# Kernel tuning notes

Hardware: AMD Instinct MI355X
Metric: run time of the kernel (lower is better)

The kernel has to match this reference:

```python
import jax, jax.numpy as jnp
import numpy as np

N, D, H, F = 50000, 128, 8, 512
HD = D // H
EPS_BN = 1e-5


def _batchnorm(x, gamma, beta):
    # BatchNorm1d in training mode: per-feature batch stats over node dim
    m = x.mean(axis=0)
    v = x.var(axis=0)
    return (x - m) * jax.lax.rsqrt(v + EPS_BN) * gamma + beta


def setup_inputs() -> dict:
    key = jax.random.key(0)
    ks = jax.random.split(key, 12)
    s = 0.05
    return {
        "src": jax.random.normal(ks[0], (N, D), jnp.float32),
        "edge_index": jax.random.randint(ks[1], (2, 800000), 0, N, jnp.int64),
        "q_w": jax.random.normal(ks[2], (D, D), jnp.float32) * s,
        "q_b": jnp.zeros((D,), jnp.float32),
        "k_w": jax.random.normal(ks[3], (D, D), jnp.float32) * s,
        "v_w": jax.random.normal(ks[4], (D, D), jnp.float32) * s,
        "out_w": jax.random.normal(ks[5], (D, D), jnp.float32) * s,
        "out_b": jnp.zeros((D,), jnp.float32),
        "g1": jnp.ones((D,), jnp.float32),
        "b1": jnp.zeros((D,), jnp.float32),
        "lin1_w": jax.random.normal(ks[6], (F, D), jnp.float32) * s,
        "lin1_b": jnp.zeros((F,), jnp.float32),
        "lin2_w": jax.random.normal(ks[7], (D, F), jnp.float32) * s,
        "lin2_b": jnp.zeros((D,), jnp.float32),
        "g2": jnp.ones((D,), jnp.float32),
        "b2": jnp.zeros((D,), jnp.float32),
    }


def reference(src, edge_index, q_w, q_b, k_w, v_w, out_w, out_b,
              g1, b1, lin1_w, lin1_b, lin2_w, lin2_b, g2, b2):
    n = src.shape[0]
    # add self loops, then attention edge index is (dst=edge[1], src=edge[0])
    loops = jnp.arange(n, dtype=edge_index.dtype)
    ei = jnp.concatenate([edge_index, jnp.stack([loops, loops])], axis=1)
    e_src, e_dst = ei[0], ei[1]  # message flows e_src -> e_dst; query index = e_dst

    scaling = float(HD) ** (-0.5)
    q = ((src @ q_w.T + q_b) * scaling).reshape(n, H, HD)
    k = (src @ k_w.T).reshape(n, H, HD)
    v = (src @ v_w.T).reshape(n, H, HD)

    # per-edge scores [E, H]
    w = jnp.einsum("ehd,ehd->eh", q[e_dst], k[e_src])
    # deterministic segment softmax over edges grouped by destination node
    mx = jax.ops.segment_max(w, e_dst, num_segments=n)
    ex = jnp.exp(w - mx[e_dst])
    den = jax.ops.segment_sum(ex, e_dst, num_segments=n)
    attn_w = ex / (den[e_dst] + 1e-16)  # [E, H]

    # weighted scatter-add aggregation -> [n, H, HD]
    msgs = attn_w[:, :, None] * v[e_src]
    agg = jax.ops.segment_sum(msgs, e_dst, num_segments=n)

    attn_out = agg.reshape(n, D) @ out_w.T + out_b
    x = _batchnorm(src + attn_out, g1, b1)

    ff = jax.nn.leaky_relu(x @ lin1_w.T + lin1_b, negative_slope=0.01)
    ff = ff @ lin2_w.T + lin2_b
    x = _batchnorm(x + ff, g2, b2)
    return x
```

## Files before the change

kernel.cpp:

```cpp
#include <hip/hip_runtime.h>
#include <math.h>

#define D 128
#define H 8
#define HD 16

typedef __attribute__((ext_vector_type(8))) short bf16x8;
typedef __attribute__((ext_vector_type(4))) float f32x4;

__device__ __forceinline__ ushort f2bf(float x) {
    union { float f; unsigned u; } v; v.f = x;
    unsigned r = v.u + 0x7fffu + ((v.u >> 16) & 1u);
    return (ushort)(r >> 16);
}
__device__ __forceinline__ float bflo(unsigned u) {
    union { unsigned u; float f; } x; x.u = u << 16; return x.f;
}
__device__ __forceinline__ float bfhi(unsigned u) {
    union { unsigned u; float f; } x; x.u = u & 0xffff0000u; return x.f;
}
__device__ __forceinline__ float bf2f(short s) {
    union { unsigned u; float f; } x; x.u = ((unsigned)(ushort)s) << 16; return x.f;
}

__device__ __forceinline__ float dot16(const float* qf, uint4 a, uint4 b) {
    float w;
    w  = qf[0]  * bflo(a.x) + qf[1]  * bfhi(a.x);
    w += qf[2]  * bflo(a.y) + qf[3]  * bfhi(a.y);
    w += qf[4]  * bflo(a.z) + qf[5]  * bfhi(a.z);
    w += qf[6]  * bflo(a.w) + qf[7]  * bfhi(a.w);
    w += qf[8]  * bflo(b.x) + qf[9]  * bfhi(b.x);
    w += qf[10] * bflo(b.y) + qf[11] * bfhi(b.y);
    w += qf[12] * bflo(b.z) + qf[13] * bfhi(b.z);
    w += qf[14] * bflo(b.w) + qf[15] * bfhi(b.w);
    return w;
}
__device__ __forceinline__ void acc16(float* num, float e, uint4 a, uint4 b) {
    num[0]  = fmaf(e, bflo(a.x), num[0]);  num[1]  = fmaf(e, bfhi(a.x), num[1]);
    num[2]  = fmaf(e, bflo(a.y), num[2]);  num[3]  = fmaf(e, bfhi(a.y), num[3]);
    num[4]  = fmaf(e, bflo(a.z), num[4]);  num[5]  = fmaf(e, bfhi(a.z), num[5]);
    num[6]  = fmaf(e, bflo(a.w), num[6]);  num[7]  = fmaf(e, bfhi(a.w), num[7]);
    num[8]  = fmaf(e, bflo(b.x), num[8]);  num[9]  = fmaf(e, bfhi(b.x), num[9]);
    num[10] = fmaf(e, bflo(b.y), num[10]); num[11] = fmaf(e, bfhi(b.y), num[11]);
    num[12] = fmaf(e, bflo(b.z), num[12]); num[13] = fmaf(e, bfhi(b.z), num[13]);
    num[14] = fmaf(e, bflo(b.w), num[14]); num[15] = fmaf(e, bfhi(b.w), num[15]);
}

template<int EPI, int M, int STATS>
__global__ __launch_bounds__(256)
void gemm_v4_kernel(const ushort* __restrict__ A,
                    const ushort* __restrict__ W,
                    const float* __restrict__ bias,
                    const float* __restrict__ extf,
                    ushort* __restrict__ outb,
                    float* __restrict__ stats,
                    int N)
{
    const int lane = threadIdx.x & 63, wave = threadIdx.x >> 6;
    const int lr = lane & 15, lq = lane >> 4;
    const int colbase = blockIdx.y * 128 + wave * 32;

    bf16x8 bfr[2][4];
    {
        const ushort* wp = W + (size_t)(colbase + lr) * 128 + lq * 8;
        #pragma unroll
        for (int ct = 0; ct < 2; ++ct)
            #pragma unroll
            for (int t = 0; t < 4; ++t)
                bfr[ct][t] = *(const bf16x8*)(wp + (size_t)ct * 16 * 128 + t * 32);
    }
    float biasv[2];
    biasv[0] = bias[colbase + lr];
    biasv[1] = bias[colbase + 16 + lr];

    float ssum[2] = {0.f, 0.f}, ssq[2] = {0.f, 0.f};

    const int stride = gridDim.x * 32;
    int r0 = blockIdx.x * 32;
    if (r0 < N) {
        bf16x8 cur[2][4], nxt[2][4];
        auto loadA = [&](int rb, bf16x8 (&dst)[2][4]) {
            #pragma unroll
            for (int s = 0; s < 2; ++s) {
                int ar = min(rb + s * 16 + lr, N - 1);
                const ushort* ap = A + (size_t)ar * 128 + lq * 8;
                #pragma unroll
                for (int t = 0; t < 4; ++t)
                    dst[s][t] = *(const bf16x8*)(ap + t * 32);
            }
        };
        loadA(r0, cur);

        while (true) {
            int rn = r0 + stride;
            if (rn < N) loadA(rn, nxt);

            f32x4 acc[2][2] = {};
            #pragma unroll
            for (int t = 0; t < 4; ++t) {
                acc[0][0] = __builtin_amdgcn_mfma_f32_16x16x32_bf16(cur[0][t], bfr[0][t], acc[0][0], 0, 0, 0);
                acc[1][0] = __builtin_amdgcn_mfma_f32_16x16x32_bf16(cur[1][t], bfr[0][t], acc[1][0], 0, 0, 0);
                acc[0][1] = __builtin_amdgcn_mfma_f32_16x16x32_bf16(cur[0][t], bfr[1][t], acc[0][1], 0, 0, 0);
                acc[1][1] = __builtin_amdgcn_mfma_f32_16x16x32_bf16(cur[1][t], bfr[1][t], acc[1][1], 0, 0, 0);
            }

            #pragma unroll
            for (int ct = 0; ct < 2; ++ct) {
                int gcol = colbase + ct * 16 + lr;
                #pragma unroll
                for (int s = 0; s < 2; ++s) {
                    #pragma unroll
                    for (int r = 0; r < 4; ++r) {
                        int grow = r0 + s * 16 + lq * 4 + r;
                        if (grow >= N) continue;
                        size_t o = (size_t)grow * M + gcol;
                        float v = acc[s][ct][r] + biasv[ct];
                        if (EPI == 2)      v = v > 0.f ? v : 0.01f * v;
                        else if (EPI == 3) v += extf[o];
                        if (STATS) { ssum[ct] += v; ssq[ct] = fmaf(v, v, ssq[ct]); }
                        outb[o] = f2bf(v);
                    }
                }
            }

            if (rn >= N) break;
            r0 = rn;
            #pragma unroll
            for (int s = 0; s < 2; ++s)
                #pragma unroll
                for (int t = 0; t < 4; ++t) cur[s][t] = nxt[s][t];
        }
    }

    if (STATS) {
        #pragma unroll
        for (int ct = 0; ct < 2; ++ct) {
            float a = ssum[ct], b = ssq[ct];
            a += __shfl_xor(a, 16, 64);  b += __shfl_xor(b, 16, 64);
            a += __shfl_xor(a, 32, 64);  b += __shfl_xor(b, 32, 64);
            if (lq == 0) {
                unsafeAtomicAdd(&stats[colbase + ct * 16 + lr], a);
                unsafeAtomicAdd(&stats[128 + colbase + ct * 16 + lr], b);
            }
        }
    }
}

#define LIN2_MFMA4(buf, kcb) \
    acc[0] = __builtin_amdgcn_mfma_f32_16x16x32_bf16(buf[0][0], bfr[(kcb)*4+0], acc[0], 0, 0, 0); \
    acc[1] = __builtin_amdgcn_mfma_f32_16x16x32_bf16(buf[1][0], bfr[(kcb)*4+0], acc[1], 0, 0, 0); \
    acc[0] = __builtin_amdgcn_mfma_f32_16x16x32_bf16(buf[0][1], bfr[(kcb)*4+1], acc[0], 0, 0, 0); \
    acc[1] = __builtin_amdgcn_mfma_f32_16x16x32_bf16(buf[1][1], bfr[(kcb)*4+1], acc[1], 0, 0, 0); \
    acc[0] = __builtin_amdgcn_mfma_f32_16x16x32_bf16(buf[0][2], bfr[(kcb)*4+2], acc[0], 0, 0, 0); \
    acc[1] = __builtin_amdgcn_mfma_f32_16x16x32_bf16(buf[1][2], bfr[(kcb)*4+2], acc[1], 0, 0, 0); \
    acc[0] = __builtin_amdgcn_mfma_f32_16x16x32_bf16(buf[0][3], bfr[(kcb)*4+3], acc[0], 0, 0, 0); \
    acc[1] = __builtin_amdgcn_mfma_f32_16x16x32_bf16(buf[1][3], bfr[(kcb)*4+3], acc[1], 0, 0, 0);

template<int GX>
__global__ __launch_bounds__(256, 3)
void lin2_kernel(const ushort* __restrict__ Ap,
                 const ushort* __restrict__ W,
                 const float* __restrict__ bias,
                 const ushort* __restrict__ extb,
                 const float* __restrict__ rawstats,
                 const float* __restrict__ gg,
                 const float* __restrict__ bb,
                 ushort* __restrict__ outb,
                 float* __restrict__ stats2,
                 int N)
{
    const int lane = threadIdx.x & 63, wave = threadIdx.x >> 6;
    const int lr = lane & 15, lq = lane >> 4;
    const int col = blockIdx.y * 64 + wave * 16 + lr;

    bf16x8 bfr[16];
    {
        const ushort* wp = W + (size_t)col * 512 + lq * 8;
        #pragma unroll
        for (int t = 0; t < 16; ++t) bfr[t] = *(const bf16x8*)(wp + t * 32);
    }
    float biasv = bias[col];
    float mean = rawstats[col] / (float)N;
    float var  = rawstats[128 + col] / (float)N - mean * mean;
    float scv  = gg[col] * rsqrtf(var + 1e-5f);
    float shv  = bb[col] - mean * scv;

    float ssum = 0.f, ssq = 0.f;

    const int stride = GX * 32;
    int r0 = blockIdx.x * 32;
    if (r0 < N) {
        bf16x8 bufA[2][4], bufB[2][4];
        auto loadA = [&](int rb, int kc, bf16x8 (&dst)[2][4]) {
            #pragma unroll
            for (int s = 0; s < 2; ++s) {
                int ar = min(rb + s * 16 + lr, N - 1);
                const ushort* ap = Ap + (size_t)ar * 512 + kc * 128 + lq * 8;
                #pragma unroll
                for (int t = 0; t < 4; ++t)
                    dst[s][t] = *(const bf16x8*)(ap + t * 32);
            }
        };
        loadA(r0, 0, bufA);
        while (true) {
            int rn = r0 + stride;
            f32x4 acc[2] = {};
            loadA(r0, 1, bufB);
            LIN2_MFMA4(bufA, 0)
            loadA(r0, 2, bufA);
            LIN2_MFMA4(bufB, 1)
            loadA(r0, 3, bufB);
            LIN2_MFMA4(bufA, 2)
            if (rn < N) loadA(rn, 0, bufA);
            LIN2_MFMA4(bufB, 3)

            #pragma unroll
            for (int s = 0; s < 2; ++s) {
                #pragma unroll
                for (int r = 0; r < 4; ++r) {
                    int grow = r0 + s * 16 + lq * 4 + r;
                    if (grow >= N) continue;
                    size_t o = (size_t)grow * 128 + col;
                    float v = acc[s][r] + biasv + fmaf(bf2f((short)extb[o]), scv, shv);
                    ssum += v;
                    ssq = fmaf(v, v, ssq);
                    outb[o] = f2bf(v);
                }
            }
            if (rn >= N) break;
            r0 = rn;
        }
    }
    ssum += __shfl_xor(ssum, 16, 64);
    ssq  += __shfl_xor(ssq, 16, 64);
    ssum += __shfl_xor(ssum, 32, 64);
    ssq  += __shfl_xor(ssq, 32, 64);
    if (lq == 0) {
        unsafeAtomicAdd(&stats2[col], ssum);
        unsafeAtomicAdd(&stats2[128 + col], ssq);
    }
}

__global__ __launch_bounds__(256)
void convert_deg_kernel(const float* __restrict__ qw, const float* __restrict__ qb,
                        const float* __restrict__ kw, const float* __restrict__ vw,
                        const float* __restrict__ ow, const float* __restrict__ w1,
                        const float* __restrict__ w2,
                        ushort* __restrict__ wqkv, ushort* __restrict__ wout,
                        ushort* __restrict__ w1b, ushort* __restrict__ w2b,
                        float* __restrict__ bqkv,
                        const float* __restrict__ src, ushort* __restrict__ srcbf,
                        int nd8,
                        const int* __restrict__ ei, long long E0,
                        int* __restrict__ deg)
{
    long long i = (long long)blockIdx.x * 256 + threadIdx.x;
    if (i < E0) atomicAdd(&deg[ei[E0 + i]], 1);
    if (i < nd8) {
        const float4* sp = (const float4*)(src + i * 8);
        float4 f0 = sp[0], f1 = sp[1];
        ushort u[8];
        u[0]=f2bf(f0.x); u[1]=f2bf(f0.y); u[2]=f2bf(f0.z); u[3]=f2bf(f0.w);
        u[4]=f2bf(f1.x); u[5]=f2bf(f1.y); u[6]=f2bf(f1.z); u[7]=f2bf(f1.w);
        *(uint4*)(srcbf + i * 8) = *(uint4*)u;
    }
    if (i < 49152) {
        int row = (int)i >> 7;
        float v;
        if (row < 128)      v = 0.25f * qw[i];
        else if (row < 256) v = kw[i - 16384];
        else                v = vw[i - 32768];
        wqkv[i] = f2bf(v);
        return;
    }
    long long j = i - 49152;
    if (j < 16384) { wout[j] = f2bf(ow[j]); return; }
    j -= 16384;
    if (j < 65536) { w1b[j] = f2bf(w1[j]); return; }
    j -= 65536;
    if (j < 65536) { w2b[j] = f2bf(w2[j]); return; }
    j -= 65536;
    if (j < 384) bqkv[j] = (j < 128) ? 0.25f * qb[j] : 0.f;
}

__global__ __launch_bounds__(256)
void w1fold_kernel(const ushort* __restrict__ w1b, const float* __restrict__ lb1,
                   const float* __restrict__ rawstats,
                   const float* __restrict__ g1, const float* __restrict__ b1,
                   ushort* __restrict__ w1f, float* __restrict__ bias1f, int N)
{
    int f = blockIdx.x * 4 + (threadIdx.x >> 6);
    int lane = threadIdx.x & 63;
    int k0 = lane * 2;
    float m0 = rawstats[k0] / (float)N;
    float v0 = rawstats[128 + k0] / (float)N - m0 * m0;
    float sc0 = g1[k0] * rsqrtf(v0 + 1e-5f);
    float sh0 = b1[k0] - m0 * sc0;
    float m1 = rawstats[k0 + 1] / (float)N;
    float v1 = rawstats[128 + k0 + 1] / (float)N - m1 * m1;
    float sc1 = g1[k0 + 1] * rsqrtf(v1 + 1e-5f);
    float sh1 = b1[k0 + 1] - m1 * sc1;

    uint wp = *(const uint*)(w1b + (size_t)f * 128 + k0);
    float w0 = bflo(wp), w1v = bfhi(wp);
    uint o = (uint)f2bf(w0 * sc0) | ((uint)f2bf(w1v * sc1) << 16);
    *(uint*)(w1f + (size_t)f * 128 + k0) = o;

    float part = w0 * sh0 + w1v * sh1;
    #pragma unroll
    for (int m = 1; m < 64; m <<= 1) part += __shfl_xor(part, m, 64);
    if (lane == 0) bias1f[f] = lb1[f] + part;
}

__global__ __launch_bounds__(256)
void scan_block_sum(const int* __restrict__ deg, int n, int* __restrict__ bsum)
{
    __shared__ int sh[256];
    int i = blockIdx.x * 256 + threadIdx.x;
    sh[threadIdx.x] = (i < n) ? deg[i] : 0;
    __syncthreads();
    for (int ofs = 128; ofs > 0; ofs >>= 1) {
        if (threadIdx.x < ofs) sh[threadIdx.x] += sh[threadIdx.x + ofs];
        __syncthreads();
    }
    if (threadIdx.x == 0) bsum[blockIdx.x] = sh[0];
}

__global__ __launch_bounds__(256)
void scan_final(const int* __restrict__ deg, int n, const int* __restrict__ bsum,
                int nb, int* __restrict__ rowptr)
{
    __shared__ int sb[256];
    __shared__ int sh[256];
    int t = threadIdx.x;
    sb[t] = (t < nb) ? bsum[t] : 0;
    __syncthreads();
    for (int ofs = 1; ofs < 256; ofs <<= 1) {
        int v = (t >= ofs) ? sb[t - ofs] : 0;
        __syncthreads();
        sb[t] += v;
        __syncthreads();
    }
    int boff = (blockIdx.x == 0) ? 0 : sb[blockIdx.x - 1];

    int i = blockIdx.x * 256 + t;
    int v = (i < n) ? deg[i] : 0;
    sh[t] = v;
    __syncthreads();
    for (int ofs = 1; ofs < 256; ofs <<= 1) {
        int u = (t >= ofs) ? sh[t - ofs] : 0;
        __syncthreads();
        sh[t] += u;
        __syncthreads();
    }
    if (i < n) rowptr[i] = boff + sh[t] - v;
    if (i == n - 1) rowptr[n] = boff + sh[t];
}

__global__ __launch_bounds__(256)
void scatter_kernel(const int* __restrict__ ei, long long E0,
                    const int* __restrict__ rowptr, int* __restrict__ cnt,
                    int* __restrict__ col)
{
    long long e = (long long)blockIdx.x * 256 + threadIdx.x;
    if (e >= E0) return;
    int s = ei[e], d = ei[E0 + e];
    int pos = rowptr[d] + atomicAdd(&cnt[d], 1);
    col[pos] = s;
}

__global__ __launch_bounds__(256)
void gat_agg_kernel(const int* __restrict__ rowptr, const int* __restrict__ col,
                    const ushort* __restrict__ qkv, ushort* __restrict__ agg, int N)
{
    int node = blockIdx.x * 4 + (threadIdx.x >> 6);
    if (node >= N) return;
    int lane = threadIdx.x & 63;
    int es = lane >> 3, h = lane & 7;
    const uint4* Q = (const uint4*)qkv;

    const uint4* qp = Q + (size_t)node * 48 + h * 2;
    uint4 qa = qp[0], qb = qp[1];
    float qf[16];
    qf[0]=bflo(qa.x); qf[1]=bfhi(qa.x); qf[2]=bflo(qa.y); qf[3]=bfhi(qa.y);
    qf[4]=bflo(qa.z); qf[5]=bfhi(qa.z); qf[6]=bflo(qa.w); qf[7]=bfhi(qa.w);
    qf[8]=bflo(qb.x); qf[9]=bfhi(qb.x); qf[10]=bflo(qb.y); qf[11]=bfhi(qb.y);
    qf[12]=bflo(qb.z); qf[13]=bfhi(qb.z); qf[14]=bflo(qb.w); qf[15]=bfhi(qb.w);

    float num[16];
    #pragma unroll
    for (int i = 0; i < 16; i++) num[i] = 0.f;
    float den = 0.f;

    int beg = rowptr[node];
    int total = rowptr[node + 1] - beg + 1;
    for (int idx = es; idx < total; idx += 8) {
        int s = (idx == 0) ? node : col[beg + idx - 1];
        const uint4* rp = Q + (size_t)s * 48 + h * 2;
        uint4 ka = rp[16], kb = rp[17], va = rp[32], vb = rp[33];
        float ev = __expf(dot16(qf, ka, kb));
        den += ev;
        acc16(num, ev, va, vb);
    }

    #pragma unroll
    for (int m = 8; m < 64; m <<= 1) {
        den += __shfl_xor(den, m, 64);
        #pragma unroll
        for (int i = 0; i < 16; i++) num[i] += __shfl_xor(num[i], m, 64);
    }

    if (es == 0) {
        float inv = 1.f / (den + 1e-16f);
        uint4 o0, o1;
        o0.x = (uint)f2bf(num[0]*inv)  | ((uint)f2bf(num[1]*inv)  << 16);
        o0.y = (uint)f2bf(num[2]*inv)  | ((uint)f2bf(num[3]*inv)  << 16);
        o0.z = (uint)f2bf(num[4]*inv)  | ((uint)f2bf(num[5]*inv)  << 16);
        o0.w = (uint)f2bf(num[6]*inv)  | ((uint)f2bf(num[7]*inv)  << 16);
        o1.x = (uint)f2bf(num[8]*inv)  | ((uint)f2bf(num[9]*inv)  << 16);
        o1.y = (uint)f2bf(num[10]*inv) | ((uint)f2bf(num[11]*inv) << 16);
        o1.z = (uint)f2bf(num[12]*inv) | ((uint)f2bf(num[13]*inv) << 16);
        o1.w = (uint)f2bf(num[14]*inv) | ((uint)f2bf(num[15]*inv) << 16);
        uint4* op = (uint4*)(agg + (size_t)node * 128 + h * 16);
        op[0] = o0; op[1] = o1;
    }
}

__global__ __launch_bounds__(256)
void bn_apply_out_kernel(const ushort* __restrict__ y, const float* __restrict__ rawstats,
                         const float* __restrict__ g, const float* __restrict__ b,
                         float* __restrict__ out, int total4, int N)
{
    __shared__ float scs[128], shs[128];
    if (threadIdx.x < 128) {
        int j = threadIdx.x;
        float mean = rawstats[j] / (float)N;
        float var  = rawstats[128 + j] / (float)N - mean * mean;
        float sc = g[j] * rsqrtf(var + 1e-5f);
        scs[j] = sc;
        shs[j] = b[j] - mean * sc;
    }
    __syncthreads();
    int i = blockIdx.x * 256 + threadIdx.x;
    if (i >= total4) return;
    uint2 u = reinterpret_cast<const uint2*>(y)[i];
    int j = (i * 4) & (D - 1);
    float4 v;
    v.x = bflo(u.x) * scs[j + 0] + shs[j + 0];
    v.y = bfhi(u.x) * scs[j + 1] + shs[j + 1];
    v.z = bflo(u.y) * scs[j + 2] + shs[j + 2];
    v.w = bfhi(u.y) * scs[j + 3] + shs[j + 3];
    reinterpret_cast<float4*>(out)[i] = v;
}

extern "C" void kernel_launch(void* const* d_in, const int* in_sizes, int n_in,
                              void* d_out, int out_size, void* d_ws, size_t ws_size,
                              hipStream_t stream)
{
    const float* src    = (const float*)d_in[0];
    const int*   ei     = (const int*)  d_in[1];
    const float* q_w    = (const float*)d_in[2];
    const float* q_b    = (const float*)d_in[3];
    const float* k_w    = (const float*)d_in[4];
    const float* v_w    = (const float*)d_in[5];
    const float* out_w  = (const float*)d_in[6];
    const float* out_b  = (const float*)d_in[7];
    const float* g1     = (const float*)d_in[8];
    const float* b1     = (const float*)d_in[9];
    const float* lin1_w = (const float*)d_in[10];
    const float* lin1_b = (const float*)d_in[11];
    const float* lin2_w = (const float*)d_in[12];
    const float* lin2_b = (const float*)d_in[13];
    const float* g2     = (const float*)d_in[14];
    const float* b2     = (const float*)d_in[15];

    const int N        = in_sizes[0] / D;
    const long long E0 = in_sizes[1] / 2;

    float* ws = (float*)d_ws;
    size_t off = 0;
    ushort* qkv   = (ushort*)(ws + off); off += (size_t)N * 192;
    ushort* agg   = (ushort*)(ws + off); off += (size_t)N * 64;
    ushort* srcbf = (ushort*)(ws + off); off += (size_t)N * 64;
    ushort* y1b   = (ushort*)(ws + off); off += (size_t)N * 64;
    ushort* hid   = (ushort*)(ws + off); off += (size_t)N * 256;
    ushort* y2b   = (ushort*)(ws + off); off += (size_t)N * 64;
    ushort* wqkv  = (ushort*)(ws + off); off += 24576;
    ushort* woutb = (ushort*)(ws + off); off += 8192;
    ushort* w1b   = (ushort*)(ws + off); off += 32768;
    ushort* w1f   = (ushort*)(ws + off); off += 32768;
    ushort* w2b   = (ushort*)(ws + off); off += 32768;
    float*  bqkv  = ws + off;            off += 384;
    float*  bias1f= ws + off;            off += 512;
    size_t zero_start = off;
    int* deg    = (int*)(ws + off); off += N;
    int* cnt    = (int*)(ws + off); off += N;
    float* stats1 = ws + off; off += 512;
    float* stats2 = ws + off; off += 512;
    size_t zero_cnt = off - zero_start;
    int* rowptr = (int*)(ws + off); off += N + 1;
    int* bsum   = (int*)(ws + off); off += 256;
    int* col    = (int*)(ws + off); off += E0;

    hipMemsetAsync(ws + zero_start, 0, zero_cnt * sizeof(float), stream);

    dim3 blk(256);

    dim3 gE0((unsigned)((E0 + 255) / 256));
    hipLaunchKernelGGL(convert_deg_kernel, gE0, blk, 0, stream,
                       q_w, q_b, k_w, v_w, out_w, lin1_w, lin2_w,
                       wqkv, woutb, w1b, w2b, bqkv,
                       src, srcbf, N * 16, ei, E0, deg);

    int nb = (N + 255) / 256;
    hipLaunchKernelGGL(scan_block_sum, dim3(nb), blk, 0, stream, deg, N, bsum);
    hipLaunchKernelGGL(scan_final, dim3(nb), blk, 0, stream, deg, N, bsum, nb, rowptr);
    hipLaunchKernelGGL(scatter_kernel, gE0, blk, 0, stream, ei, E0, rowptr, cnt, col);

    const int gx = 1024;

    hipLaunchKernelGGL((gemm_v4_kernel<0, 384, 0>), dim3(gx, 3), blk, 0, stream,
                       srcbf, wqkv, bqkv, nullptr, qkv, nullptr, N);

    hipLaunchKernelGGL(gat_agg_kernel, dim3((N + 3) / 4), blk, 0, stream,
                       rowptr, col, qkv, agg, N);

    hipLaunchKernelGGL((gemm_v4_kernel<3, 128, 1>), dim3(gx, 1), blk, 0, stream,
                       agg, woutb, out_b, src, y1b, stats1, N);

    hipLaunchKernelGGL(w1fold_kernel, dim3(128), blk, 0, stream,
                       w1b, lin1_b, stats1, g1, b1, w1f, bias1f, N);

    hipLaunchKernelGGL((gemm_v4_kernel<2, 512, 0>), dim3(gx, 4), blk, 0, stream,
                       y1b, w1f, bias1f, nullptr, hid, nullptr, N);

    hipLaunchKernelGGL((lin2_kernel<512>), dim3(512, 2), blk, 0, stream,
                       hid, w2b, lin2_b, y1b, stats1, g1, b1, y2b, stats2, N);

    int total4 = N * D / 4;
    hipLaunchKernelGGL(bn_apply_out_kernel, dim3((total4 + 255) / 256), blk, 0, stream,
                       y2b, stats2, g2, b2, (float*)d_out, total4, N);
}
```

Baseline: 448.6 us.

## Fuse FFN lin1 and lin2 GEMMs into one kernel keeping hidden in registers

Replaces the separate lin1 GEMM, which wrote a bf16 hidden tensor of size N×512, and the lin2 kernel with a single fused kernel. Each wave takes 32 rows, computes 32-wide hidden slices with MFMA, applies bias and leaky ReLU, repacks the result to bf16 with permlane swaps, and feeds it straight into the lin2 MFMAs. The BN1 residual, BN2 statistics and output write are folded into the epilogue. This removes the hidden tensor round trip through HBM and one launch, but each wave now reloads the W1 and W2 fragments from global memory or cache, and register pressure is higher (64 accumulator VGPRs per wave, occupancy bound of 2).

After: 545.7 us. 21.6% more time.

```diff
diff --git a/kernel.cpp b/kernel.cpp
--- a/kernel.cpp
+++ b/kernel.cpp
@@ -146,98 +146,153 @@
     }
 }
 
-#define LIN2_MFMA4(buf, kcb) \
-    acc[0] = __builtin_amdgcn_mfma_f32_16x16x32_bf16(buf[0][0], bfr[(kcb)*4+0], acc[0], 0, 0, 0); \
-    acc[1] = __builtin_amdgcn_mfma_f32_16x16x32_bf16(buf[1][0], bfr[(kcb)*4+0], acc[1], 0, 0, 0); \
-    acc[0] = __builtin_amdgcn_mfma_f32_16x16x32_bf16(buf[0][1], bfr[(kcb)*4+1], acc[0], 0, 0, 0); \
-    acc[1] = __builtin_amdgcn_mfma_f32_16x16x32_bf16(buf[1][1], bfr[(kcb)*4+1], acc[1], 0, 0, 0); \
-    acc[0] = __builtin_amdgcn_mfma_f32_16x16x32_bf16(buf[0][2], bfr[(kcb)*4+2], acc[0], 0, 0, 0); \
-    acc[1] = __builtin_amdgcn_mfma_f32_16x16x32_bf16(buf[1][2], bfr[(kcb)*4+2], acc[1], 0, 0, 0); \
-    acc[0] = __builtin_amdgcn_mfma_f32_16x16x32_bf16(buf[0][3], bfr[(kcb)*4+3], acc[0], 0, 0, 0); \
-    acc[1] = __builtin_amdgcn_mfma_f32_16x16x32_bf16(buf[1][3], bfr[(kcb)*4+3], acc[1], 0, 0, 0);
-
-template<int GX>
-__global__ __launch_bounds__(256, 3)
-void lin2_kernel(const ushort* __restrict__ Ap,
-                 const ushort* __restrict__ W,
-                 const float* __restrict__ bias,
-                 const ushort* __restrict__ extb,
-                 const float* __restrict__ rawstats,
-                 const float* __restrict__ gg,
-                 const float* __restrict__ bb,
-                 ushort* __restrict__ outb,
-                 float* __restrict__ stats2,
-                 int N)
-{
+__global__ __launch_bounds__(256, 2)
+void ffn_fused_kernel(const ushort* __restrict__ y1b,
+                      const ushort* __restrict__ w1f,
+                      const float*  __restrict__ bias1f,
+                      const ushort* __restrict__ w2b,
+                      const float*  __restrict__ lb2,
+                      const float*  __restrict__ rawstats,
+                      const float*  __restrict__ g1b,
+                      const float*  __restrict__ b1b,
+                      ushort* __restrict__ y2b,
+                      float*  __restrict__ stats2,
+                      int N)
+{
+    __shared__ float scs[128], adv[128], b1s[512];
+    {
+        int t = threadIdx.x;
+        if (t < 128) {
+            float mean = rawstats[t] / (float)N;
+            float var  = rawstats[128 + t] / (float)N - mean * mean;
+            float sc = g1b[t] * rsqrtf(var + 1e-5f);
+            scs[t] = sc;
+            adv[t] = lb2[t] + b1b[t] - mean * sc;
+        }
+        b1s[t] = bias1f[t];
+        b1s[t + 256] = bias1f[t + 256];
+    }
+    __syncthreads();
+
     const int lane = threadIdx.x & 63, wave = threadIdx.x >> 6;
     const int lr = lane & 15, lq = lane >> 4;
-    const int col = blockIdx.y * 64 + wave * 16 + lr;
-
-    bf16x8 bfr[16];
-    {
-        const ushort* wp = W + (size_t)col * 512 + lq * 8;
-        #pragma unroll
-        for (int t = 0; t < 16; ++t) bfr[t] = *(const bf16x8*)(wp + t * 32);
-    }
-    float biasv = bias[col];
-    float mean = rawstats[col] / (float)N;
-    float var  = rawstats[128 + col] / (float)N - mean * mean;
-    float scv  = gg[col] * rsqrtf(var + 1e-5f);
-    float shv  = bb[col] - mean * scv;
-
-    float ssum = 0.f, ssq = 0.f;
-
-    const int stride = GX * 32;
-    int r0 = blockIdx.x * 32;
-    if (r0 < N) {
-        bf16x8 bufA[2][4], bufB[2][4];
-        auto loadA = [&](int rb, int kc, bf16x8 (&dst)[2][4]) {
-            #pragma unroll
-            for (int s = 0; s < 2; ++s) {
-                int ar = min(rb + s * 16 + lr, N - 1);
-                const ushort* ap = Ap + (size_t)ar * 512 + kc * 128 + lq * 8;
-                #pragma unroll
-                for (int t = 0; t < 4; ++t)
-                    dst[s][t] = *(const bf16x8*)(ap + t * 32);
-            }
-        };
-        loadA(r0, 0, bufA);
-        while (true) {
-            int rn = r0 + stride;
-            f32x4 acc[2] = {};
-            loadA(r0, 1, bufB);
-            LIN2_MFMA4(bufA, 0)
-            loadA(r0, 2, bufA);
-            LIN2_MFMA4(bufB, 1)
-            loadA(r0, 3, bufB);
-            LIN2_MFMA4(bufA, 2)
-            if (rn < N) loadA(rn, 0, bufA);
-            LIN2_MFMA4(bufB, 3)
-
-            #pragma unroll
-            for (int s = 0; s < 2; ++s) {
-                #pragma unroll
-                for (int r = 0; r < 4; ++r) {
-                    int grow = r0 + s * 16 + lq * 4 + r;
-                    if (grow >= N) continue;
-                    size_t o = (size_t)grow * 128 + col;
-                    float v = acc[s][r] + biasv + fmaf(bf2f((short)extb[o]), scv, shv);
-                    ssum += v;
-                    ssq = fmaf(v, v, ssq);
-                    outb[o] = f2bf(v);
-                }
-            }
-            if (rn >= N) break;
-            r0 = rn;
-        }
-    }
-    ssum += __shfl_xor(ssum, 16, 64);
-    ssq  += __shfl_xor(ssq, 16, 64);
-    ssum += __shfl_xor(ssum, 32, 64);
-    ssq  += __shfl_xor(ssq, 32, 64);
-    if (lq == 0) {
-        unsafeAtomicAdd(&stats2[col], ssum);
-        unsafeAtomicAdd(&stats2[128 + col], ssq);
+    const int chunk = blockIdx.x * 4 + wave;
+    const int r0 = chunk * 32;
+    if (r0 >= N) return;
+
+    bf16x8 yfr[2][4];
+    #pragma unroll
+    for (int s = 0; s < 2; ++s) {
+        int ar = min(r0 + s * 16 + lr, N - 1);
+        const ushort* ap = y1b + (size_t)ar * 128 + lq * 8;
+        #pragma unroll
+        for (int t = 0; t < 4; ++t) yfr[s][t] = *(const bf16x8*)(ap + t * 32);
+    }
+
+    f32x4 acc[8][2] = {};
+
+    auto loadW1 = [&](int u, bf16x8 (&w1d)[2][4], float4 (&bad)[2]) {
+        const ushort* wp = w1f + (size_t)(u * 32 + lr) * 128 + lq * 8;
+        #pragma unroll
+        for (int t = 0; t < 4; ++t) {
+            w1d[0][t] = *(const bf16x8*)(wp + t * 32);
+            w1d[1][t] = *(const bf16x8*)(wp + 16 * 128 + t * 32);
+        }
+        bad[0] = *(const float4*)&b1s[u * 32 + lq * 4];
+        bad[1] = *(const float4*)&b1s[u * 32 + 16 + lq * 4];
+    };
+
+    auto computeU = [&](int u, bf16x8 (&w1fr)[2][4], float4 (&bav)[2]) {
+        bf16x8 w2fr[8];
+        const ushort* wp2 = w2b + (size_t)lr * 512 + u * 32 + lq * 8;
+        #pragma unroll
+        for (int c = 0; c < 8; ++c)
+            w2fr[c] = *(const bf16x8*)(wp2 + (size_t)c * 16 * 512);
+
+        #pragma unroll
+        for (int s = 0; s < 2; ++s) {
+            f32x4 h0 = {}, h1 = {};
+            #pragma unroll
+            for (int t = 0; t < 4; ++t) {
+                h0 = __builtin_amdgcn_mfma_f32_16x16x32_bf16(w1fr[0][t], yfr[s][t], h0, 0, 0, 0);
+                h1 = __builtin_amdgcn_mfma_f32_16x16x32_bf16(w1fr[1][t], yfr[s][t], h1, 0, 0, 0);
+            }
+            float p[8];
+            p[0] = h0[0] + bav[0].x; p[1] = h0[1] + bav[0].y;
+            p[2] = h0[2] + bav[0].z; p[3] = h0[3] + bav[0].w;
+            p[4] = h1[0] + bav[1].x; p[5] = h1[1] + bav[1].y;
+            p[6] = h1[2] + bav[1].z; p[7] = h1[3] + bav[1].w;
+            #pragma unroll
+            for (int i = 0; i < 8; ++i) p[i] = p[i] > 0.f ? p[i] : 0.01f * p[i];
+
+            uint w0, w1_, w2_, w3_;
+            asm("v_cvt_pk_bf16_f32 %0, %1, %2" : "=v"(w0)  : "v"(p[0]), "v"(p[1]));
+            asm("v_cvt_pk_bf16_f32 %0, %1, %2" : "=v"(w1_) : "v"(p[2]), "v"(p[3]));
+            asm("v_cvt_pk_bf16_f32 %0, %1, %2" : "=v"(w2_) : "v"(p[4]), "v"(p[5]));
+            asm("v_cvt_pk_bf16_f32 %0, %1, %2" : "=v"(w3_) : "v"(p[6]), "v"(p[7]));
+            asm("v_permlane32_swap_b32 %0, %1" : "+v"(w0),  "+v"(w2_));
+            asm("v_permlane16_swap_b32 %0, %1" : "+v"(w0),  "+v"(w2_));
+            asm("v_permlane32_swap_b32 %0, %1" : "+v"(w1_), "+v"(w3_));
+            asm("v_permlane16_swap_b32 %0, %1" : "+v"(w1_), "+v"(w3_));
+            union { uint u4[4]; bf16x8 v; } pk;
+            pk.u4[0] = w0; pk.u4[1] = w1_; pk.u4[2] = w2_; pk.u4[3] = w3_;
+
+            #pragma unroll
+            for (int c = 0; c < 8; ++c)
+                acc[c][s] = __builtin_amdgcn_mfma_f32_16x16x32_bf16(w2fr[c], pk.v, acc[c][s], 0, 0, 0);
+        }
+    };
+
+    bf16x8 w1A[2][4], w1B[2][4];
+    float4 baA[2], baB[2];
+    loadW1(0, w1A, baA);
+    #pragma unroll 1
+    for (int u = 0; u < 16; u += 2) {
+        loadW1(u + 1, w1B, baB);
+        computeU(u, w1A, baA);
+        if (u < 14) loadW1(u + 2, w1A, baA);
+        computeU(u + 1, w1B, baB);
+    }
+
+    #pragma unroll
+    for (int ct2 = 0; ct2 < 8; ++ct2) {
+        int cb = ct2 * 16 + lq * 4;
+        float4 sc4 = *(const float4*)&scs[cb];
+        float4 ad4 = *(const float4*)&adv[cb];
+        float ts[4] = {0.f, 0.f, 0.f, 0.f}, tq[4] = {0.f, 0.f, 0.f, 0.f};
+        #pragma unroll
+        for (int s = 0; s < 2; ++s) {
+            int grow = r0 + s * 16 + lr;
+            bool ok = grow < N;
+            int gr = ok ? grow : N - 1;
+            ushort4 rv = *(const ushort4*)(y1b + (size_t)gr * 128 + cb);
+            float o0 = acc[ct2][s][0] + ad4.x + bf2f((short)rv.x) * sc4.x;
+            float o1 = acc[ct2][s][1] + ad4.y + bf2f((short)rv.y) * sc4.y;
+            float o2 = acc[ct2][s][2] + ad4.z + bf2f((short)rv.z) * sc4.z;
+            float o3 = acc[ct2][s][3] + ad4.w + bf2f((short)rv.w) * sc4.w;
+            if (ok) {
+                ts[0] += o0; tq[0] = fmaf(o0, o0, tq[0]);
+                ts[1] += o1; tq[1] = fmaf(o1, o1, tq[1]);
+                ts[2] += o2; tq[2] = fmaf(o2, o2, tq[2]);
+                ts[3] += o3; tq[3] = fmaf(o3, o3, tq[3]);
+                uint2 st;
+                st.x = (uint)f2bf(o0) | ((uint)f2bf(o1) << 16);
+                st.y = (uint)f2bf(o2) | ((uint)f2bf(o3) << 16);
+                *(uint2*)(y2b + (size_t)grow * 128 + cb) = st;
+            }
+        }
+        #pragma unroll
+        for (int r = 0; r < 4; ++r) {
+            float a = ts[r], q = tq[r];
+            a += __shfl_xor(a, 1, 64);  q += __shfl_xor(q, 1, 64);
+            a += __shfl_xor(a, 2, 64);  q += __shfl_xor(q, 2, 64);
+            a += __shfl_xor(a, 4, 64);  q += __shfl_xor(q, 4, 64);
+            a += __shfl_xor(a, 8, 64);  q += __shfl_xor(q, 8, 64);
+            if (lr == 0) {
+                unsafeAtomicAdd(&stats2[cb + r], a);
+                unsafeAtomicAdd(&stats2[128 + cb + r], q);
+            }
+        }
     }
 }
 
@@ -483,7 +538,6 @@
     ushort* agg   = (ushort*)(ws + off); off += (size_t)N * 64;
     ushort* srcbf = (ushort*)(ws + off); off += (size_t)N * 64;
     ushort* y1b   = (ushort*)(ws + off); off += (size_t)N * 64;
-    ushort* hid   = (ushort*)(ws + off); off += (size_t)N * 256;
     ushort* y2b   = (ushort*)(ws + off); off += (size_t)N * 64;
     ushort* wqkv  = (ushort*)(ws + off); off += 24576;
     ushort* woutb = (ushort*)(ws + off); off += 8192;
@@ -531,11 +585,10 @@
     hipLaunchKernelGGL(w1fold_kernel, dim3(128), blk, 0, stream,
                        w1b, lin1_b, stats1, g1, b1, w1f, bias1f, N);
 
-    hipLaunchKernelGGL((gemm_v4_kernel<2, 512, 0>), dim3(gx, 4), blk, 0, stream,
-                       y1b, w1f, bias1f, nullptr, hid, nullptr, N);
-
-    hipLaunchKernelGGL((lin2_kernel<512>), dim3(512, 2), blk, 0, stream,
-                       hid, w2b, lin2_b, y1b, stats1, g1, b1, y2b, stats2, N);
+    int nchunks = (N + 31) / 32;
+    hipLaunchKernelGGL(ffn_fused_kernel, dim3((nchunks + 3) / 4), blk, 0, stream,
+                       y1b, w1f, bias1f, w2b, lin2_b, stats1, g1, b1,
+                       y2b, stats2, N);
 
     int total4 = N * D / 4;
     hipLaunchKernelGGL(bn_apply_out_kernel, dim3((total4 + 255) / 256), blk, 0, stream,
```
